# Performance work log

Hardware: AMD Instinct MI355X
Metric: run time of the kernel (lower is better)

Reference implementation:

```python
import jax, jax.numpy as jnp
import numpy as np
from jax import lax

B, S, H = 4, 512, 2048
E, D = 16, 128
GH = E * D  # GRU hidden size = num_experts * router_dim
BAL_STRENGTH = 0.01


def _l2norm(v, eps):
    n = jnp.linalg.norm(v, axis=-1, keepdims=True)
    return v / jnp.maximum(n, eps)


def setup_inputs() -> dict:
    key = jax.random.key(0)
    ks = jax.random.split(key, 6)
    x = jax.random.normal(ks[0], (B, S, H), dtype=jnp.float32)
    hn = jax.random.normal(ks[1], (1, B, GH), dtype=jnp.float32)
    w_ih = jax.random.normal(ks[2], (3 * GH, H), dtype=jnp.float32) * 0.02
    w_hh = jax.random.normal(ks[3], (3 * GH, GH), dtype=jnp.float32) * 0.02
    w_expr = jax.random.normal(ks[4], (H, GH), dtype=jnp.float32) * 0.02
    expert_load_ema = jax.random.uniform(ks[5], (E,), dtype=jnp.float32)
    return {"x": x, "hn": hn, "w_ih": w_ih, "w_hh": w_hh,
            "w_expr": w_expr, "expert_load_ema": expert_load_ema, "top_k": 2}


def _gru(x, h0, w_ih, w_hh):
    # PyTorch GRU (no bias): gates ordered (r, z, n). Precompute input proj once.
    xi = jnp.einsum('bsh,gh->sbg', x, w_ih)  # [S,B,3*GH]
    xr, xz, xn = jnp.split(xi, 3, axis=-1)
    wr, wz, wn = jnp.split(w_hh, 3, axis=0)

    def step(h, xs):
        xr_t, xz_t, xn_t = xs
        r = jax.nn.sigmoid(xr_t + h @ wr.T)
        z = jax.nn.sigmoid(xz_t + h @ wz.T)
        n = jnp.tanh(xn_t + r * (h @ wn.T))
        h = (1.0 - z) * n + z * h
        return h, h

    hT, hs = lax.scan(step, h0, (xr, xz, xn))
    return hs.transpose(1, 0, 2), hT[None]  # [B,S,GH], [1,B,GH]


def reference(x, hn, w_ih, w_hh, w_expr, expert_load_ema, top_k):
    b, s, _ = x.shape
    e = expert_load_ema.shape[0]
    gh = w_hh.shape[1]
    d = gh // e

    routing_logits, hn_out = _gru(x, hn[0], w_ih, w_hh)

    expression_logits = (x @ w_expr).reshape(b, s, e, d)
    rout = routing_logits.reshape(b, s, e, d)
    rout = _l2norm(rout, 1e-12)  # F.normalize(dim=-1)

    # per-token expert gram matrix [B,S,E,E]
    gram = jnp.einsum('bsed,bsfd->bsef', rout, rout)
    diff = gram - jnp.eye(e, dtype=rout.dtype)
    diffn = _l2norm(diff, 1e-12)
    speciality_penalty = jnp.mean(jnp.sum(diffn ** 2, axis=(-2, -1)))

    # cosine sim (rout already unit-norm)
    en = jnp.maximum(jnp.linalg.norm(expression_logits, axis=-1), 1e-8)
    rn = jnp.maximum(jnp.linalg.norm(rout, axis=-1), 1e-8)
    cos = jnp.sum(expression_logits * rout, axis=-1) / (en * rn)
    cosine_similarities = 1.0 - cos  # [B,S,E]

    domain = (cosine_similarities * (1.0 + speciality_penalty)).reshape(b * s, e)
    top_vals, selected_experts = lax.top_k(domain, top_k)
    multiplier = jax.nn.softmax(top_vals.astype(jnp.float32), axis=-1).astype(domain.dtype)

    # ExpressionProjector orthogonal loss
    gw = w_expr.T @ w_expr
    expression_loss = jnp.mean((gw - jnp.eye(gh, dtype=w_expr.dtype)) ** 2)

    # training-mode EMA load-balance adjustment (no_grad in torch)
    ema = lax.stop_gradient(expert_load_ema)
    total = ema.sum()
    scores = jnp.where(total > 0, ema / jnp.maximum(total, 1e-12), jnp.zeros_like(ema))
    adjustment = scores * BAL_STRENGTH * e
    multiplier = multiplier - adjustment[selected_experts]

    return (multiplier, selected_experts, expression_logits, hn_out,
            speciality_penalty, cosine_similarities, expression_loss)
```

## Files before the change

### kernel.cpp

```cpp
#include <hip/hip_runtime.h>
#include <hip/hip_bf16.h>
#include <math.h>

#define BB 4
#define SS 512
#define HH 2048
#define EE 16
#define DD 128
#define GH 2048
#define G3 6144
#define NTOK 2048

#define LSTR 132
#define FPAD 32
#define KS 40

typedef __attribute__((ext_vector_type(8))) short short8;
typedef __attribute__((ext_vector_type(4))) float f32x4;

__global__ __launch_bounds__(256) void gemm_abt(const float* __restrict__ A,
                                                const float* __restrict__ B,
                                                float* __restrict__ C,
                                                int M, int N, int K) {
  __shared__ float As[8][LSTR];
  __shared__ float Bs[8][LSTR];
  const int bm = blockIdx.y * 128, bn = blockIdx.x * 128;
  const int tid = threadIdx.x;
  const int lm = tid >> 1;
  const int kh = (tid & 1) * 4;
  const int tx = tid & 15, ty = tid >> 4;
  float acc[8][8] = {};
  const float* Arow = A + (size_t)(bm + lm) * K + kh;
  const float* Brow = B + (size_t)(bn + lm) * K + kh;
  for (int k0 = 0; k0 < K; k0 += 8) {
    float4 av = *(const float4*)(Arow + k0);
    float4 bv = *(const float4*)(Brow + k0);
    As[kh + 0][lm] = av.x; As[kh + 1][lm] = av.y; As[kh + 2][lm] = av.z; As[kh + 3][lm] = av.w;
    Bs[kh + 0][lm] = bv.x; Bs[kh + 1][lm] = bv.y; Bs[kh + 2][lm] = bv.z; Bs[kh + 3][lm] = bv.w;
    __syncthreads();
#pragma unroll
    for (int kk = 0; kk < 8; ++kk) {
      float a8[8], b8[8];
      *(float4*)(a8)     = *(const float4*)(&As[kk][ty * 8]);
      *(float4*)(a8 + 4) = *(const float4*)(&As[kk][ty * 8 + 4]);
      *(float4*)(b8)     = *(const float4*)(&Bs[kk][tx * 8]);
      *(float4*)(b8 + 4) = *(const float4*)(&Bs[kk][tx * 8 + 4]);
#pragma unroll
      for (int i = 0; i < 8; ++i)
#pragma unroll
        for (int j = 0; j < 8; ++j) acc[i][j] = fmaf(a8[i], b8[j], acc[i][j]);
    }
    __syncthreads();
  }
#pragma unroll
  for (int i = 0; i < 8; ++i) {
    float4 v0 = {acc[i][0], acc[i][1], acc[i][2], acc[i][3]};
    float4 v1 = {acc[i][4], acc[i][5], acc[i][6], acc[i][7]};
    float* crow = C + (size_t)(bm + ty * 8 + i) * N + bn + tx * 8;
    *(float4*)(crow)     = v0;
    *(float4*)(crow + 4) = v1;
  }
}

__global__ __launch_bounds__(256) void gemm_ab(const float* __restrict__ A,
                                               const float* __restrict__ B,
                                               float* __restrict__ C,
                                               int M, int N, int K) {
  __shared__ float As[8][LSTR];
  __shared__ float Bs[8][LSTR];
  const int bm = blockIdx.y * 128, bn = blockIdx.x * 128;
  const int tid = threadIdx.x;
  const int lm = tid >> 1;
  const int kh = (tid & 1) * 4;
  const int bk = tid >> 5;
  const int bn4 = (tid & 31) * 4;
  const int tx = tid & 15, ty = tid >> 4;
  float acc[8][8] = {};
  const float* Arow = A + (size_t)(bm + lm) * K + kh;
  for (int k0 = 0; k0 < K; k0 += 8) {
    float4 av = *(const float4*)(Arow + k0);
    float4 bv = *(const float4*)(B + (size_t)(k0 + bk) * N + bn + bn4);
    As[kh + 0][lm] = av.x; As[kh + 1][lm] = av.y; As[kh + 2][lm] = av.z; As[kh + 3][lm] = av.w;
    *(float4*)(&Bs[bk][bn4]) = bv;
    __syncthreads();
#pragma unroll
    for (int kk = 0; kk < 8; ++kk) {
      float a8[8], b8[8];
      *(float4*)(a8)     = *(const float4*)(&As[kk][ty * 8]);
      *(float4*)(a8 + 4) = *(const float4*)(&As[kk][ty * 8 + 4]);
      *(float4*)(b8)     = *(const float4*)(&Bs[kk][tx * 8]);
      *(float4*)(b8 + 4) = *(const float4*)(&Bs[kk][tx * 8 + 4]);
#pragma unroll
      for (int i = 0; i < 8; ++i)
#pragma unroll
        for (int j = 0; j < 8; ++j) acc[i][j] = fmaf(a8[i], b8[j], acc[i][j]);
    }
    __syncthreads();
  }
#pragma unroll
  for (int i = 0; i < 8; ++i) {
    float4 v0 = {acc[i][0], acc[i][1], acc[i][2], acc[i][3]};
    float4 v1 = {acc[i][4], acc[i][5], acc[i][6], acc[i][7]};
    float* crow = C + (size_t)(bm + ty * 8 + i) * N + bn + tx * 8;
    *(float4*)(crow)     = v0;
    *(float4*)(crow + 4) = v1;
  }
}

__global__ __launch_bounds__(256) void ata_loss(const float* __restrict__ A,
                                                float* __restrict__ el_accum,
                                                int N, int K) {
  __shared__ float As[8][LSTR];
  __shared__ float Bs[8][LSTR];
  __shared__ float red[256];
  const int bi = blockIdx.y * 128, bj = blockIdx.x * 128;
  const int tid = threadIdx.x;
  const int bk = tid >> 5;
  const int bn4 = (tid & 31) * 4;
  const int tx = tid & 15, ty = tid >> 4;
  float acc[8][8] = {};
  for (int k0 = 0; k0 < K; k0 += 8) {
    float4 av = *(const float4*)(A + (size_t)(k0 + bk) * N + bi + bn4);
    float4 bv = *(const float4*)(A + (size_t)(k0 + bk) * N + bj + bn4);
    *(float4*)(&As[bk][bn4]) = av;
    *(float4*)(&Bs[bk][bn4]) = bv;
    __syncthreads();
#pragma unroll
    for (int kk = 0; kk < 8; ++kk) {
      float a8[8], b8[8];
      *(float4*)(a8)     = *(const float4*)(&As[kk][ty * 8]);
      *(float4*)(a8 + 4) = *(const float4*)(&As[kk][ty * 8 + 4]);
      *(float4*)(b8)     = *(const float4*)(&Bs[kk][tx * 8]);
      *(float4*)(b8 + 4) = *(const float4*)(&Bs[kk][tx * 8 + 4]);
#pragma unroll
      for (int i = 0; i < 8; ++i)
#pragma unroll
        for (int j = 0; j < 8; ++j) acc[i][j] = fmaf(a8[i], b8[j], acc[i][j]);
    }
    __syncthreads();
  }
  float local = 0.f;
#pragma unroll
  for (int i = 0; i < 8; ++i) {
#pragma unroll
    for (int j = 0; j < 8; ++j) {
      int gi = bi + ty * 8 + i, gj = bj + tx * 8 + j;
      float d = acc[i][j] - ((gi == gj) ? 1.0f : 0.0f);
      local += d * d;
    }
  }
  red[tid] = local;
  __syncthreads();
  for (int s = 128; s > 0; s >>= 1) {
    if (tid < s) red[tid] += red[tid + s];
    __syncthreads();
  }
  if (tid == 0) atomicAdd(el_accum, red[0]);
}

__device__ inline void bf16_split(float v, unsigned short& hi, unsigned short& lo) {
  unsigned u = __float_as_uint(v);
  unsigned r = u + 0x7FFFu + ((u >> 16) & 1u);
  hi = (unsigned short)(r >> 16);
  float rem = v - __uint_as_float((unsigned)hi << 16);
  lo = (unsigned short)(__float_as_uint(rem) >> 16);
}

__global__ __launch_bounds__(256) void split_mat(const float* __restrict__ A,
                                                 unsigned short* __restrict__ Hh,
                                                 unsigned short* __restrict__ Hl,
                                                 int n) {
  int i = blockIdx.x * 256 + threadIdx.x;
  int stride = gridDim.x * 256;
  for (; i < n; i += stride) {
    unsigned short hi, lo;
    bf16_split(A[i], hi, lo);
    Hh[i] = hi; Hl[i] = lo;
  }
}

__global__ __launch_bounds__(256) void transpose_split(const float* __restrict__ A,
                                                       unsigned short* __restrict__ Th,
                                                       unsigned short* __restrict__ Tl) {
  __shared__ float tile[64][65];
  const int bx = blockIdx.x * 64, by = blockIdx.y * 64;
  const int tx = threadIdx.x & 63, ty = threadIdx.x >> 6;
#pragma unroll
  for (int i = 0; i < 16; ++i) {
    int r = ty + i * 4;
    tile[r][tx] = A[(size_t)(by + r) * GH + bx + tx];
  }
  __syncthreads();
#pragma unroll
  for (int i = 0; i < 16; ++i) {
    int r = ty + i * 4;
    unsigned short hi, lo;
    bf16_split(tile[tx][r], hi, lo);
    Th[(size_t)(bx + r) * HH + by + tx] = hi;
    Tl[(size_t)(bx + r) * HH + by + tx] = lo;
  }
}

__global__ __launch_bounds__(256) void gemm_abt_bf16(
    const unsigned short* __restrict__ Ah, const unsigned short* __restrict__ Al,
    const unsigned short* __restrict__ Bh, const unsigned short* __restrict__ Bl,
    float* __restrict__ C, int M, int N, int K) {
  __shared__ unsigned short Ahs[128 * KS], Als[128 * KS];
  __shared__ unsigned short Bhs[128 * KS], Bls[128 * KS];
  const int tid = threadIdx.x;
  const int wv = tid >> 6, lane = tid & 63;
  const int qr = wv >> 1, qc = wv & 1;
  const int m16 = lane & 15, q = lane >> 4;
  const int bm = blockIdx.y * 128, bn = blockIdx.x * 128;
  const int sr = tid >> 1, sh = (tid & 1) * 16;
  f32x4 zero = {0.f, 0.f, 0.f, 0.f};
  f32x4 acc[4][4];
#pragma unroll
  for (int i = 0; i < 4; ++i)
#pragma unroll
    for (int j = 0; j < 4; ++j) acc[i][j] = zero;

  for (int k0 = 0; k0 < K; k0 += 32) {
    const size_t ga = (size_t)(bm + sr) * K + k0 + sh;
    const size_t gb = (size_t)(bn + sr) * K + k0 + sh;
    short8 a0 = *(const short8*)(Ah + ga);
    short8 a1 = *(const short8*)(Ah + ga + 8);
    short8 l0 = *(const short8*)(Al + ga);
    short8 l1 = *(const short8*)(Al + ga + 8);
    short8 b0 = *(const short8*)(Bh + gb);
    short8 b1 = *(const short8*)(Bh + gb + 8);
    short8 m0 = *(const short8*)(Bl + gb);
    short8 m1 = *(const short8*)(Bl + gb + 8);
    __syncthreads();
    *(short8*)&Ahs[sr * KS + sh]     = a0;
    *(short8*)&Ahs[sr * KS + sh + 8] = a1;
    *(short8*)&Als[sr * KS + sh]     = l0;
    *(short8*)&Als[sr * KS + sh + 8] = l1;
    *(short8*)&Bhs[sr * KS + sh]     = b0;
    *(short8*)&Bhs[sr * KS + sh + 8] = b1;
    *(short8*)&Bls[sr * KS + sh]     = m0;
    *(short8*)&Bls[sr * KS + sh + 8] = m1;
    __syncthreads();
    short8 afh[4], afl[4], bfh[4], bfl[4];
#pragma unroll
    for (int t = 0; t < 4; ++t) {
      const int raddr = (qr * 64 + t * 16 + m16) * KS + q * 8;
      const int caddr = (qc * 64 + t * 16 + m16) * KS + q * 8;
      afh[t] = *(const short8*)&Ahs[raddr];
      afl[t] = *(const short8*)&Als[raddr];
      bfh[t] = *(const short8*)&Bhs[caddr];
      bfl[t] = *(const short8*)&Bls[caddr];
    }
#pragma unroll
    for (int tm = 0; tm < 4; ++tm)
#pragma unroll
      for (int tn = 0; tn < 4; ++tn) {
        acc[tm][tn] = __builtin_amdgcn_mfma_f32_16x16x32_bf16(afh[tm], bfh[tn], acc[tm][tn], 0, 0, 0);
        acc[tm][tn] = __builtin_amdgcn_mfma_f32_16x16x32_bf16(afh[tm], bfl[tn], acc[tm][tn], 0, 0, 0);
        acc[tm][tn] = __builtin_amdgcn_mfma_f32_16x16x32_bf16(afl[tm], bfh[tn], acc[tm][tn], 0, 0, 0);
      }
  }
#pragma unroll
  for (int tm = 0; tm < 4; ++tm)
#pragma unroll
    for (int tn = 0; tn < 4; ++tn)
#pragma unroll
      for (int r = 0; r < 4; ++r)
        C[(size_t)(bm + qr * 64 + tm * 16 + q * 4 + r) * N +
          bn + qc * 64 + tn * 16 + m16] = acc[tm][tn][r];
}

__global__ __launch_bounds__(256) void ata_bf16(
    const unsigned short* __restrict__ Th, const unsigned short* __restrict__ Tl,
    float* __restrict__ el_accum, int N, int K) {
  __shared__ unsigned short Ahs[128 * KS], Als[128 * KS];
  __shared__ unsigned short Bhs[128 * KS], Bls[128 * KS];
  __shared__ float red[256];
  const int tid = threadIdx.x;
  const int wv = tid >> 6, lane = tid & 63;
  const int qr = wv >> 1, qc = wv & 1;
  const int m16 = lane & 15, q = lane >> 4;
  const int bi = blockIdx.y * 128, bj = blockIdx.x * 128;
  const int sr = tid >> 1, sh = (tid & 1) * 16;
  f32x4 zero = {0.f, 0.f, 0.f, 0.f};
  f32x4 acc[4][4];
#pragma unroll
  for (int i = 0; i < 4; ++i)
#pragma unroll
    for (int j = 0; j < 4; ++j) acc[i][j] = zero;

  for (int k0 = 0; k0 < K; k0 += 32) {
    const size_t ga = (size_t)(bi + sr) * K + k0 + sh;
    const size_t gb = (size_t)(bj + sr) * K + k0 + sh;
    short8 a0 = *(const short8*)(Th + ga);
    short8 a1 = *(const short8*)(Th + ga + 8);
    short8 l0 = *(const short8*)(Tl + ga);
    short8 l1 = *(const short8*)(Tl + ga + 8);
    short8 b0 = *(const short8*)(Th + gb);
    short8 b1 = *(const short8*)(Th + gb + 8);
    short8 m0 = *(const short8*)(Tl + gb);
    short8 m1 = *(const short8*)(Tl + gb + 8);
    __syncthreads();
    *(short8*)&Ahs[sr * KS + sh]     = a0;
    *(short8*)&Ahs[sr * KS + sh + 8] = a1;
    *(short8*)&Als[sr * KS + sh]     = l0;
    *(short8*)&Als[sr * KS + sh + 8] = l1;
    *(short8*)&Bhs[sr * KS + sh]     = b0;
    *(short8*)&Bhs[sr * KS + sh + 8] = b1;
    *(short8*)&Bls[sr * KS + sh]     = m0;
    *(short8*)&Bls[sr * KS + sh + 8] = m1;
    __syncthreads();
    short8 afh[4], afl[4], bfh[4], bfl[4];
#pragma unroll
    for (int t = 0; t < 4; ++t) {
      const int raddr = (qr * 64 + t * 16 + m16) * KS + q * 8;
      const int caddr = (qc * 64 + t * 16 + m16) * KS + q * 8;
      afh[t] = *(const short8*)&Ahs[raddr];
      afl[t] = *(const short8*)&Als[raddr];
      bfh[t] = *(const short8*)&Bhs[caddr];
      bfl[t] = *(const short8*)&Bls[caddr];
    }
#pragma unroll
    for (int tm = 0; tm < 4; ++tm)
#pragma unroll
      for (int tn = 0; tn < 4; ++tn) {
        acc[tm][tn] = __builtin_amdgcn_mfma_f32_16x16x32_bf16(afh[tm], bfh[tn], acc[tm][tn], 0, 0, 0);
        acc[tm][tn] = __builtin_amdgcn_mfma_f32_16x16x32_bf16(afh[tm], bfl[tn], acc[tm][tn], 0, 0, 0);
        acc[tm][tn] = __builtin_amdgcn_mfma_f32_16x16x32_bf16(afl[tm], bfh[tn], acc[tm][tn], 0, 0, 0);
      }
  }
  float local = 0.f;
#pragma unroll
  for (int tm = 0; tm < 4; ++tm)
#pragma unroll
    for (int tn = 0; tn < 4; ++tn)
#pragma unroll
      for (int r = 0; r < 4; ++r) {
        int gi = bi + qr * 64 + tm * 16 + q * 4 + r;
        int gj = bj + qc * 64 + tn * 16 + m16;
        float d = acc[tm][tn][r] - ((gi == gj) ? 1.0f : 0.0f);
        local += d * d;
      }
  red[tid] = local;
  __syncthreads();
  for (int s = 128; s > 0; s >>= 1) {
    if (tid < s) red[tid] += red[tid + s];
    __syncthreads();
  }
  if (tid == 0) atomicAdd(el_accum, red[0]);
}

template <int CTRL>
__device__ inline float dpp_add(float v) {
  int t = __builtin_amdgcn_update_dpp(0, __float_as_int(v), CTRL, 0xf, 0xf, false);
  return v + __int_as_float(t);
}
__device__ inline float wred_l63(float v) {
  v = dpp_add<0x111>(v);
  v = dpp_add<0x112>(v);
  v = dpp_add<0x114>(v);
  v = dpp_add<0x118>(v);
  v = dpp_add<0x142>(v);
  v = dpp_add<0x143>(v);
  return v;
}

__global__ __launch_bounds__(640) void gru_persistent(
    const float* __restrict__ xi,
    const float* __restrict__ w_hh,
    const float* __restrict__ hn,
    float* __restrict__ hsx,
    int* __restrict__ flags) {
  __shared__ __align__(16) float hsm[2][BB * GH];
  __shared__ int arrive_cnt;
  __shared__ int ready_cnt;
  const int tid = threadIdx.x;
  const int wave = tid >> 6, lane = tid & 63;

  if (tid == 0) { arrive_cnt = 0; ready_cnt = 0; }
  if (tid < 512) {
#pragma unroll
    for (int i = 0; i < 4; ++i) {
      int k = tid + i * 512;
      float4 v;
      v.x = hn[0 * GH + k]; v.y = hn[1 * GH + k];
      v.z = hn[2 * GH + k]; v.w = hn[3 * GH + k];
      int slot = k ^ ((k >> 3) & 3);
      *(float4*)(&hsm[0][slot * 4]) = v;
    }
  }
  __syncthreads();

  if (wave < 8) {
    const int j = blockIdx.x * 8 + wave;
    float wgr[32], wgz[32], wgn[32];
    {
      const float* pr = w_hh + (size_t)j * GH;
      const float* pz = w_hh + (size_t)(GH + j) * GH;
      const float* pn = w_hh + (size_t)(2 * GH + j) * GH;
#pragma unroll
      for (int c = 0; c < 32; ++c) {
        int k = c * 64 + lane;
        wgr[c] = pr[k]; wgz[c] = pz[k]; wgn[c] = pn[k];
      }
    }
    const int rdo = (lane ^ ((lane >> 3) & 3)) * 4;
    const int hpo = (j ^ ((j >> 3) & 3)) * 4;

    for (int s = 0; s < SS; ++s) {
      float xr[BB], xz[BB], xn_[BB];
      if (lane == 63) {
#pragma unroll
        for (int b = 0; b < BB; ++b) {
          const float* xrow = xi + ((size_t)(b * SS + s)) * G3;
          xr[b]  = xrow[j];
          xz[b]  = xrow[GH + j];
          xn_[b] = xrow[2 * GH + j];
        }
      }
      if (s > 0) {
        const int want = 128 * s;
        while (__hip_atomic_load(&ready_cnt, __ATOMIC_ACQUIRE,
                                 __HIP_MEMORY_SCOPE_WORKGROUP) < want)
          __builtin_amdgcn_s_sleep(1);
      }
      const float* cur = hsm[s & 1];

      float ar[BB] = {}, az[BB] = {}, an[BB] = {};
#pragma unroll
      for (int c = 0; c < 32; ++c) {
        float4 h4 = *(const float4*)(&cur[c * 256 + rdo]);
        float w_r = wgr[c], w_z = wgz[c], w_n = wgn[c];
        ar[0] = fmaf(w_r, h4.x, ar[0]); az[0] = fmaf(w_z, h4.x, az[0]); an[0] = fmaf(w_n, h4.x, an[0]);
        ar[1] = fmaf(w_r, h4.y, ar[1]); az[1] = fmaf(w_z, h4.y, az[1]); an[1] = fmaf(w_n, h4.y, an[1]);
        ar[2] = fmaf(w_r, h4.z, ar[2]); az[2] = fmaf(w_z, h4.z, az[2]); an[2] = fmaf(w_n, h4.z, an[2]);
        ar[3] = fmaf(w_r, h4.w, ar[3]); az[3] = fmaf(w_z, h4.w, az[3]); an[3] = fmaf(w_n, h4.w, an[3]);
      }
#pragma unroll
      for (int b = 0; b < BB; ++b) {
        ar[b] = wred_l63(ar[b]); az[b] = wred_l63(az[b]); an[b] = wred_l63(an[b]);
      }

      if (lane == 63) {
        float4 hp4 = *(const float4*)(&cur[hpo]);
        float hpv[BB] = {hp4.x, hp4.y, hp4.z, hp4.w};
#pragma unroll
        for (int b = 0; b < BB; ++b) {
          float r = 1.0f / (1.0f + expf(-(xr[b] + ar[b])));
          float z = 1.0f / (1.0f + expf(-(xz[b] + az[b])));
          float n = tanhf(xn_[b] + r * an[b]);
          float hv = (1.0f - z) * n + z * hpv[b];
          __hip_atomic_store(hsx + ((size_t)s * 256 + blockIdx.x) * 32 + b * 8 + (j & 7),
                             hv, __ATOMIC_RELAXED, __HIP_MEMORY_SCOPE_AGENT);
        }
      }
      if (s + 1 < SS) {
        asm volatile("s_waitcnt vmcnt(0)" ::: "memory");
        if (lane == 63) {
          int old = __hip_atomic_fetch_add(&arrive_cnt, 1, __ATOMIC_ACQ_REL,
                                           __HIP_MEMORY_SCOPE_WORKGROUP);
          if (old == 8 * (s + 1) - 1)
            __hip_atomic_store(&flags[blockIdx.x * FPAD], s + 1,
                               __ATOMIC_RELAXED, __HIP_MEMORY_SCOPE_AGENT);
        }
      }
    }
  } else {
    const int f = tid - 512;
    int cp[4], cc4[4], ws0[4], ws1[4], ws2[4], ws3[4];
#pragma unroll
    for (int i = 0; i < 4; ++i) {
      int c = f + i * 128;
      cp[i]  = c >> 1;
      cc4[i] = (c & 1) * 4;
      int k0 = c * 4;
      ws0[i] = ((k0 + 0) ^ (((k0 + 0) >> 3) & 3)) * 4;
      ws1[i] = ((k0 + 1) ^ (((k0 + 1) >> 3) & 3)) * 4;
      ws2[i] = ((k0 + 2) ^ (((k0 + 2) >> 3) & 3)) * 4;
      ws3[i] = ((k0 + 3) ^ (((k0 + 3) >> 3) & 3)) * 4;
    }
    for (int r = 0; r + 1 < SS; ++r) {
      float* nb = hsm[(r + 1) & 1];
      const int want = r + 1;
      unsigned done = 0;
      while (done != 0xFu) {
#pragma unroll
        for (int i = 0; i < 4; ++i) {
          if (!(done & (1u << i)) &&
              __hip_atomic_load(&flags[cp[i] * FPAD], __ATOMIC_RELAXED,
                                __HIP_MEMORY_SCOPE_AGENT) >= want) {
            const float* line = hsx + ((size_t)r * 256 + cp[i]) * 32 + cc4[i];
            float4 v0 = *(const float4*)(line + 0);
            float4 v1 = *(const float4*)(line + 8);
            float4 v2 = *(const float4*)(line + 16);
            float4 v3 = *(const float4*)(line + 24);
            *(float4*)(&nb[ws0[i]]) = float4{v0.x, v1.x, v2.x, v3.x};
            *(float4*)(&nb[ws1[i]]) = float4{v0.y, v1.y, v2.y, v3.y};
            *(float4*)(&nb[ws2[i]]) = float4{v0.z, v1.z, v2.z, v3.z};
            *(float4*)(&nb[ws3[i]]) = float4{v0.w, v1.w, v2.w, v3.w};
            done |= 1u << i;
          }
        }
        if (done != 0xFu) __builtin_amdgcn_s_sleep(1);
      }
      __hip_atomic_fetch_add(&ready_cnt, 1, __ATOMIC_RELEASE,
                             __HIP_MEMORY_SCOPE_WORKGROUP);
    }
  }
}

__device__ inline float red16(float v) {
#pragma unroll
  for (int o = 8; o; o >>= 1) v += __shfl_xor(v, o);
  return v;
}

__global__ __launch_bounds__(256) void token_kernel(const float* __restrict__ hsx,
                                                    const float* __restrict__ expr,
                                                    float* __restrict__ cos_out,
                                                    float* __restrict__ sp_accum) {
  __shared__ float routn[EE * 132];
  __shared__ float rowc[EE];
  const int t = blockIdx.x;
  const int b = t / SS, s = t % SS;
  const int tid = threadIdx.x;
  const int e = tid >> 4, sub = tid & 15;

  const float* rrow = hsx + ((size_t)s * 256 + e * 16 + sub) * 32 + b * 8;
  float rv[8];
  *(float4*)(rv)     = *(const float4*)(rrow);
  *(float4*)(rv + 4) = *(const float4*)(rrow + 4);
  float ss = 0.f;
#pragma unroll
  for (int i = 0; i < 8; ++i) ss += rv[i] * rv[i];
  ss = red16(ss);
  float inv = 1.0f / fmaxf(sqrtf(ss), 1e-12f);
#pragma unroll
  for (int i = 0; i < 8; ++i) {
    rv[i] *= inv;
    routn[e * 132 + sub * 8 + i] = rv[i];
  }

  const float* erow = expr + (size_t)t * GH + e * DD + sub * 8;
  float en2 = 0.f, dot = 0.f;
#pragma unroll
  for (int i = 0; i < 8; ++i) {
    float ev = erow[i];
    en2 += ev * ev;
    dot += ev * rv[i];
  }
  en2 = red16(en2);
  dot = red16(dot);
  if (sub == 0) {
    float cosv = dot / fmaxf(sqrtf(en2), 1e-8f);
    cos_out[t * EE + e] = 1.0f - cosv;
  }
  __syncthreads();

  const int f = sub;
  float g = 0.f;
#pragma unroll
  for (int d = 0; d < DD; ++d)
    g = fmaf(routn[e * 132 + d], routn[f * 132 + d], g);
  float diff = g - ((e == f) ? 1.0f : 0.0f);
  float rowsum = red16(diff * diff);
  if (f == 0) {
    float nrm = fmaxf(sqrtf(rowsum), 1e-12f);
    rowc[e] = rowsum / (nrm * nrm);
  }
  __syncthreads();
  if (tid == 0) {
    float tok = 0.f;
#pragma unroll
    for (int i = 0; i < EE; ++i) tok += rowc[i];
    atomicAdd(sp_accum, tok);
  }
}

__global__ __launch_bounds__(256) void final_kernel(const float* __restrict__ hsx,
                                                    const float* __restrict__ cos_out,
                                                    const float* __restrict__ ema,
                                                    const float* __restrict__ accum,
                                                    float* __restrict__ out_mult,
                                                    float* __restrict__ out_sel,
                                                    float* __restrict__ out_hn,
                                                    float* __restrict__ out_sp,
                                                    float* __restrict__ out_el) {
  const int gtid = blockIdx.x * 256 + threadIdx.x;
  if (gtid < BB * GH) {
    int b = gtid / GH, k = gtid % GH;
    out_hn[gtid] = hsx[((size_t)(SS - 1) * 256 + (k >> 3)) * 32 + b * 8 + (k & 7)];
  }
  if (gtid < NTOK) {
    float sp = accum[0] / (float)NTOK;
    float scale = 1.0f + sp;
    float dv[EE];
#pragma unroll
    for (int e = 0; e < EE; ++e) dv[e] = cos_out[gtid * EE + e] * scale;
    int i0 = 0; float v0 = dv[0];
#pragma unroll
    for (int e = 1; e < EE; ++e) { if (dv[e] > v0) { v0 = dv[e]; i0 = e; } }
    int i1 = -1; float v1 = -1e30f;
#pragma unroll
    for (int e = 0; e < EE; ++e) { if (e != i0 && dv[e] > v1) { v1 = dv[e]; i1 = e; } }
    float ex = expf(v1 - v0);
    float den = 1.0f + ex;
    float m0 = 1.0f / den, m1 = ex / den;
    float total = 0.f;
#pragma unroll
    for (int e = 0; e < EE; ++e) total += ema[e];
    float a0 = 0.f, a1 = 0.f;
    if (total > 0.f) {
      float invt = 1.0f / fmaxf(total, 1e-12f);
      a0 = ema[i0] * invt * 0.01f * (float)EE;
      a1 = ema[i1] * invt * 0.01f * (float)EE;
    }
    out_mult[gtid * 2 + 0] = m0 - a0;
    out_mult[gtid * 2 + 1] = m1 - a1;
    out_sel[gtid * 2 + 0] = (float)i0;
    out_sel[gtid * 2 + 1] = (float)i1;
  }
  if (gtid == 0) {
    out_sp[0] = accum[0] / (float)NTOK;
    out_el[0] = accum[1] / (float)(GH * GH);
  }
}

extern "C" void kernel_launch(void* const* d_in, const int* in_sizes, int n_in,
                              void* d_out, int out_size, void* d_ws, size_t ws_size,
                              hipStream_t stream) {
  const float* x      = (const float*)d_in[0];
  const float* hn     = (const float*)d_in[1];
  const float* w_ih   = (const float*)d_in[2];
  const float* w_hh   = (const float*)d_in[3];
  const float* w_expr = (const float*)d_in[4];
  const float* ema    = (const float*)d_in[5];
  float* out = (float*)d_out;

  float* out_mult = out;
  float* out_sel  = out + 4096;
  float* out_expr = out + 8192;
  float* out_hn   = out + 4202496;
  float* out_sp   = out + 4210688;
  float* out_cos  = out + 4210689;
  float* out_el   = out + 4243457;

  float* ws = (float*)d_ws;
  float* xi    = ws;
  float* hsx   = ws + 12582912;
  float* accum = ws + 16777216;
  int*   flags = (int*)(ws + 16777220);
  unsigned short* xh  = (unsigned short*)(ws + 16785920);
  unsigned short* xl  = (unsigned short*)(ws + 18883072);
  unsigned short* wth = (unsigned short*)(ws + 20980224);
  unsigned short* wtl = (unsigned short*)(ws + 23077376);
  const size_t need_bytes = (size_t)25174528 * 4;
  const bool bf16path = ws_size >= need_bytes;

  hipMemsetAsync(accum, 0, (4 + 256 * FPAD) * sizeof(float), stream);

  gemm_abt<<<dim3(G3 / 128, NTOK / 128), 256, 0, stream>>>(x, w_ih, xi, NTOK, G3, HH);

  if (bf16path) {
    split_mat<<<4096, 256, 0, stream>>>(x, xh, xl, NTOK * HH);
    transpose_split<<<dim3(GH / 64, HH / 64), 256, 0, stream>>>(w_expr, wth, wtl);
    gemm_abt_bf16<<<dim3(GH / 128, NTOK / 128), 256, 0, stream>>>(
        xh, xl, wth, wtl, out_expr, NTOK, GH, HH);
    ata_bf16<<<dim3(GH / 128, GH / 128), 256, 0, stream>>>(wth, wtl, accum + 1, GH, HH);
  } else {
    gemm_ab<<<dim3(GH / 128, NTOK / 128), 256, 0, stream>>>(x, w_expr, out_expr, NTOK, GH, HH);
    ata_loss<<<dim3(GH / 128, GH / 128), 256, 0, stream>>>(w_expr, accum + 1, GH, HH);
  }

  {
    void* args[] = {(void*)&xi, (void*)&w_hh, (void*)&hn, (void*)&hsx, (void*)&flags};
    hipLaunchCooperativeKernel((void*)gru_persistent, dim3(256), dim3(640),
                               args, 0, stream);
  }

  token_kernel<<<NTOK, 256, 0, stream>>>(hsx, out_expr, out_cos, accum);

  final_kernel<<<(BB * GH + 255) / 256, 256, 0, stream>>>(hsx, out_cos, ema, accum,
                                                          out_mult, out_sel, out_hn,
                                                          out_sp, out_el);
}
```

Measured before the change: 3.989 ms.

## Pipeline GRU recurrence per batch element with per-batch flags and buffers

The persistent GRU kernel now handles the four batch rows as separate staggered pipelines. Each has its own shared-memory hidden buffer, arrive/ready counters and global flags, so batch b+1's matvec can overlap the cross-block exchange for batch b. The hidden-state exchange layout in the workspace changes to [s][b][block][8], and the token and final kernels are updated to match. The cost is four times as many flag waits and sync points per step, plus single-buffered shared memory per batch, which adds waits and may add latency.

Measured after the change: 6.121 ms. +53.5%, slower.

```diff
diff --git a/kernel.cpp b/kernel.cpp
--- a/kernel.cpp
+++ b/kernel.cpp
@@ -371,41 +371,30 @@
     const float* __restrict__ hn,
     float* __restrict__ hsx,
     int* __restrict__ flags) {
-  __shared__ __align__(16) float hsm[2][BB * GH];
-  __shared__ int arrive_cnt;
-  __shared__ int ready_cnt;
+  __shared__ __align__(16) float hsm[BB][GH];
+  __shared__ int arrive_cnt[BB];
+  __shared__ int ready_cnt[BB];
   const int tid = threadIdx.x;
   const int wave = tid >> 6, lane = tid & 63;
 
-  if (tid == 0) { arrive_cnt = 0; ready_cnt = 0; }
+  if (tid < BB) { arrive_cnt[tid] = 0; ready_cnt[tid] = 0; }
   if (tid < 512) {
 #pragma unroll
-    for (int i = 0; i < 4; ++i) {
-      int k = tid + i * 512;
-      float4 v;
-      v.x = hn[0 * GH + k]; v.y = hn[1 * GH + k];
-      v.z = hn[2 * GH + k]; v.w = hn[3 * GH + k];
-      int slot = k ^ ((k >> 3) & 3);
-      *(float4*)(&hsm[0][slot * 4]) = v;
-    }
+    for (int b = 0; b < BB; ++b)
+      *(float4*)(&hsm[b][tid * 4]) = *(const float4*)(&hn[b * GH + tid * 4]);
   }
   __syncthreads();
 
   if (wave < 8) {
     const int j = blockIdx.x * 8 + wave;
-    float wgr[32], wgz[32], wgn[32];
-    {
-      const float* pr = w_hh + (size_t)j * GH;
-      const float* pz = w_hh + (size_t)(GH + j) * GH;
-      const float* pn = w_hh + (size_t)(2 * GH + j) * GH;
-#pragma unroll
-      for (int c = 0; c < 32; ++c) {
-        int k = c * 64 + lane;
-        wgr[c] = pr[k]; wgz[c] = pz[k]; wgn[c] = pn[k];
-      }
-    }
-    const int rdo = (lane ^ ((lane >> 3) & 3)) * 4;
-    const int hpo = (j ^ ((j >> 3) & 3)) * 4;
+    float4 wgr4[8], wgz4[8], wgn4[8];
+#pragma unroll
+    for (int c = 0; c < 8; ++c) {
+      const int k = c * 256 + lane * 4;
+      wgr4[c] = *(const float4*)(w_hh + (size_t)j * GH + k);
+      wgz4[c] = *(const float4*)(w_hh + (size_t)(GH + j) * GH + k);
+      wgn4[c] = *(const float4*)(w_hh + (size_t)(2 * GH + j) * GH + k);
+    }
 
     for (int s = 0; s < SS; ++s) {
       float xr[BB], xz[BB], xn_[BB];
@@ -418,93 +407,92 @@
           xn_[b] = xrow[2 * GH + j];
         }
       }
-      if (s > 0) {
-        const int want = 128 * s;
-        while (__hip_atomic_load(&ready_cnt, __ATOMIC_ACQUIRE,
-                                 __HIP_MEMORY_SCOPE_WORKGROUP) < want)
-          __builtin_amdgcn_s_sleep(1);
-      }
-      const float* cur = hsm[s & 1];
-
-      float ar[BB] = {}, az[BB] = {}, an[BB] = {};
-#pragma unroll
-      for (int c = 0; c < 32; ++c) {
-        float4 h4 = *(const float4*)(&cur[c * 256 + rdo]);
-        float w_r = wgr[c], w_z = wgz[c], w_n = wgn[c];
-        ar[0] = fmaf(w_r, h4.x, ar[0]); az[0] = fmaf(w_z, h4.x, az[0]); an[0] = fmaf(w_n, h4.x, an[0]);
-        ar[1] = fmaf(w_r, h4.y, ar[1]); az[1] = fmaf(w_z, h4.y, az[1]); an[1] = fmaf(w_n, h4.y, an[1]);
-        ar[2] = fmaf(w_r, h4.z, ar[2]); az[2] = fmaf(w_z, h4.z, az[2]); an[2] = fmaf(w_n, h4.z, an[2]);
-        ar[3] = fmaf(w_r, h4.w, ar[3]); az[3] = fmaf(w_z, h4.w, az[3]); an[3] = fmaf(w_n, h4.w, an[3]);
-      }
 #pragma unroll
       for (int b = 0; b < BB; ++b) {
-        ar[b] = wred_l63(ar[b]); az[b] = wred_l63(az[b]); an[b] = wred_l63(an[b]);
-      }
-
-      if (lane == 63) {
-        float4 hp4 = *(const float4*)(&cur[hpo]);
-        float hpv[BB] = {hp4.x, hp4.y, hp4.z, hp4.w};
-#pragma unroll
-        for (int b = 0; b < BB; ++b) {
-          float r = 1.0f / (1.0f + expf(-(xr[b] + ar[b])));
-          float z = 1.0f / (1.0f + expf(-(xz[b] + az[b])));
-          float n = tanhf(xn_[b] + r * an[b]);
-          float hv = (1.0f - z) * n + z * hpv[b];
-          __hip_atomic_store(hsx + ((size_t)s * 256 + blockIdx.x) * 32 + b * 8 + (j & 7),
-                             hv, __ATOMIC_RELAXED, __HIP_MEMORY_SCOPE_AGENT);
+        if (s > 0) {
+          const int want = 128 * s;
+          while (__hip_atomic_load(&ready_cnt[b], __ATOMIC_ACQUIRE,
+                                   __HIP_MEMORY_SCOPE_WORKGROUP) < want)
+            __builtin_amdgcn_s_sleep(1);
+        }
+        float ar = 0.f, az = 0.f, an = 0.f;
+#pragma unroll
+        for (int c = 0; c < 8; ++c) {
+          float4 h4 = *(const float4*)(&hsm[b][c * 256 + lane * 4]);
+          float4 wr = wgr4[c], wz = wgz4[c], wn = wgn4[c];
+          ar = fmaf(wr.x, h4.x, ar); ar = fmaf(wr.y, h4.y, ar);
+          ar = fmaf(wr.z, h4.z, ar); ar = fmaf(wr.w, h4.w, ar);
+          az = fmaf(wz.x, h4.x, az); az = fmaf(wz.y, h4.y, az);
+          az = fmaf(wz.z, h4.z, az); az = fmaf(wz.w, h4.w, az);
+          an = fmaf(wn.x, h4.x, an); an = fmaf(wn.y, h4.y, an);
+          an = fmaf(wn.z, h4.z, an); an = fmaf(wn.w, h4.w, an);
+        }
+        ar = wred_l63(ar); az = wred_l63(az); an = wred_l63(an);
+
+        if (lane == 63) {
+          float hp = hsm[b][j];
+          float r = 1.0f / (1.0f + expf(-(xr[b] + ar)));
+          float z = 1.0f / (1.0f + expf(-(xz[b] + az)));
+          float n = tanhf(xn_[b] + r * an);
+          float hv = (1.0f - z) * n + z * hp;
+          __hip_atomic_store(
+              hsx + (((size_t)s * BB + b) * 256 + blockIdx.x) * 8 + (j & 7),
+              hv, __ATOMIC_RELAXED, __HIP_MEMORY_SCOPE_AGENT);
+        }
+        if (s + 1 < SS) {
+          asm volatile("s_waitcnt vmcnt(0)" ::: "memory");
+          if (lane == 63) {
+            int old = __hip_atomic_fetch_add(&arrive_cnt[b], 1, __ATOMIC_ACQ_REL,
+                                             __HIP_MEMORY_SCOPE_WORKGROUP);
+            if (old == 8 * (s + 1) - 1)
+              __hip_atomic_store(&flags[(b * 256 + blockIdx.x) * FPAD], s + 1,
+                                 __ATOMIC_RELAXED, __HIP_MEMORY_SCOPE_AGENT);
+          }
         }
       }
-      if (s + 1 < SS) {
-        asm volatile("s_waitcnt vmcnt(0)" ::: "memory");
-        if (lane == 63) {
-          int old = __hip_atomic_fetch_add(&arrive_cnt, 1, __ATOMIC_ACQ_REL,
-                                           __HIP_MEMORY_SCOPE_WORKGROUP);
-          if (old == 8 * (s + 1) - 1)
-            __hip_atomic_store(&flags[blockIdx.x * FPAD], s + 1,
-                               __ATOMIC_RELAXED, __HIP_MEMORY_SCOPE_AGENT);
-        }
-      }
     }
   } else {
     const int f = tid - 512;
-    int cp[4], cc4[4], ws0[4], ws1[4], ws2[4], ws3[4];
-#pragma unroll
-    for (int i = 0; i < 4; ++i) {
-      int c = f + i * 128;
-      cp[i]  = c >> 1;
-      cc4[i] = (c & 1) * 4;
-      int k0 = c * 4;
-      ws0[i] = ((k0 + 0) ^ (((k0 + 0) >> 3) & 3)) * 4;
-      ws1[i] = ((k0 + 1) ^ (((k0 + 1) >> 3) & 3)) * 4;
-      ws2[i] = ((k0 + 2) ^ (((k0 + 2) >> 3) & 3)) * 4;
-      ws3[i] = ((k0 + 3) ^ (((k0 + 3) >> 3) & 3)) * 4;
-    }
+    int p[4];
+#pragma unroll
+    for (int i = 0; i < 4; ++i) p[i] = (f >> 1) + i * 64;
+    const int co = (f & 1) * 4;
+
     for (int r = 0; r + 1 < SS; ++r) {
-      float* nb = hsm[(r + 1) & 1];
-      const int want = r + 1;
-      unsigned done = 0;
-      while (done != 0xFu) {
-#pragma unroll
-        for (int i = 0; i < 4; ++i) {
-          if (!(done & (1u << i)) &&
-              __hip_atomic_load(&flags[cp[i] * FPAD], __ATOMIC_RELAXED,
-                                __HIP_MEMORY_SCOPE_AGENT) >= want) {
-            const float* line = hsx + ((size_t)r * 256 + cp[i]) * 32 + cc4[i];
-            float4 v0 = *(const float4*)(line + 0);
-            float4 v1 = *(const float4*)(line + 8);
-            float4 v2 = *(const float4*)(line + 16);
-            float4 v3 = *(const float4*)(line + 24);
-            *(float4*)(&nb[ws0[i]]) = float4{v0.x, v1.x, v2.x, v3.x};
-            *(float4*)(&nb[ws1[i]]) = float4{v0.y, v1.y, v2.y, v3.y};
-            *(float4*)(&nb[ws2[i]]) = float4{v0.z, v1.z, v2.z, v3.z};
-            *(float4*)(&nb[ws3[i]]) = float4{v0.w, v1.w, v2.w, v3.w};
-            done |= 1u << i;
+#pragma unroll
+      for (int b = 0; b < BB; ++b) {
+        while (__hip_atomic_load(&arrive_cnt[b], __ATOMIC_ACQUIRE,
+                                 __HIP_MEMORY_SCOPE_WORKGROUP) < 8 * (r + 1))
+          __builtin_amdgcn_s_sleep(1);
+        const int want = r + 1;
+        unsigned done = 0;
+        while (done != 0xFu) {
+#pragma unroll
+          for (int i = 0; i < 4; ++i) {
+            if (!(done & (1u << i)) &&
+                __hip_atomic_load(&flags[(b * 256 + p[i]) * FPAD],
+                                  __ATOMIC_RELAXED,
+                                  __HIP_MEMORY_SCOPE_AGENT) >= want) {
+              const unsigned long long* seg = (const unsigned long long*)(
+                  hsx + (((size_t)r * BB + b) * 256 + p[i]) * 8 + co);
+              unsigned long long q0 = __hip_atomic_load(
+                  seg + 0, __ATOMIC_RELAXED, __HIP_MEMORY_SCOPE_AGENT);
+              unsigned long long q1 = __hip_atomic_load(
+                  seg + 1, __ATOMIC_RELAXED, __HIP_MEMORY_SCOPE_AGENT);
+              float4 v;
+              v.x = __uint_as_float((unsigned)q0);
+              v.y = __uint_as_float((unsigned)(q0 >> 32));
+              v.z = __uint_as_float((unsigned)q1);
+              v.w = __uint_as_float((unsigned)(q1 >> 32));
+              *(float4*)(&hsm[b][f * 4 + i * 512]) = v;
+              done |= 1u << i;
+            }
           }
+          if (done != 0xFu) __builtin_amdgcn_s_sleep(1);
         }
-        if (done != 0xFu) __builtin_amdgcn_s_sleep(1);
+        __hip_atomic_fetch_add(&ready_cnt[b], 1, __ATOMIC_RELEASE,
+                               __HIP_MEMORY_SCOPE_WORKGROUP);
       }
-      __hip_atomic_fetch_add(&ready_cnt, 1, __ATOMIC_RELEASE,
-                             __HIP_MEMORY_SCOPE_WORKGROUP);
     }
   }
 }
@@ -526,7 +514,7 @@
   const int tid = threadIdx.x;
   const int e = tid >> 4, sub = tid & 15;
 
-  const float* rrow = hsx + ((size_t)s * 256 + e * 16 + sub) * 32 + b * 8;
+  const float* rrow = hsx + (((size_t)s * BB + b) * 256 + e * 16 + sub) * 8;
   float rv[8];
   *(float4*)(rv)     = *(const float4*)(rrow);
   *(float4*)(rv + 4) = *(const float4*)(rrow + 4);
@@ -589,7 +577,8 @@
   const int gtid = blockIdx.x * 256 + threadIdx.x;
   if (gtid < BB * GH) {
     int b = gtid / GH, k = gtid % GH;
-    out_hn[gtid] = hsx[((size_t)(SS - 1) * 256 + (k >> 3)) * 32 + b * 8 + (k & 7)];
+    out_hn[gtid] =
+        hsx[(((size_t)(SS - 1) * BB + b) * 256 + (k >> 3)) * 8 + (k & 7)];
   }
   if (gtid < NTOK) {
     float sp = accum[0] / (float)NTOK;
@@ -650,14 +639,14 @@
   float* hsx   = ws + 12582912;
   float* accum = ws + 16777216;
   int*   flags = (int*)(ws + 16777220);
-  unsigned short* xh  = (unsigned short*)(ws + 16785920);
-  unsigned short* xl  = (unsigned short*)(ws + 18883072);
-  unsigned short* wth = (unsigned short*)(ws + 20980224);
-  unsigned short* wtl = (unsigned short*)(ws + 23077376);
-  const size_t need_bytes = (size_t)25174528 * 4;
+  unsigned short* xh  = (unsigned short*)(ws + 16810240);
+  unsigned short* xl  = (unsigned short*)(ws + 18907392);
+  unsigned short* wth = (unsigned short*)(ws + 21004544);
+  unsigned short* wtl = (unsigned short*)(ws + 23101696);
+  const size_t need_bytes = (size_t)25198848 * 4;
   const bool bf16path = ws_size >= need_bytes;
 
-  hipMemsetAsync(accum, 0, (4 + 256 * FPAD) * sizeof(float), stream);
+  hipMemsetAsync(accum, 0, (4 + 4 * 256 * FPAD) * sizeof(float), stream);
 
   gemm_abt<<<dim3(G3 / 128, NTOK / 128), 256, 0, stream>>>(x, w_ih, xi, NTOK, G3, HH);
 
```
